# Kernel optimization log

Measured on AMD Instinct MI355X. Metric: run time of the kernel, lower is better.

## Reference

```python
import jax, jax.numpy as jnp
import numpy as np

T, B, D, H, NQ = 512, 256, 256, 256, 4  # note H == B is required by the original torch broadcasting


def setup_inputs() -> dict:
    key = jax.random.key(0)
    ks = jax.random.split(key, 9)
    inp = {"inputs": jax.random.normal(ks[0], (T, B, D), jnp.float32)}
    names = ["forget", "input", "update", "output"]
    for j, n in enumerate(names):
        inp[f"W_{n}"] = jax.random.normal(ks[1 + j], (NQ, D + H), jnp.float32) * 0.05
        inp[f"b_{n}"] = jnp.zeros((NQ,), jnp.float32)
        inp[f"phi_{n}"] = jax.random.uniform(ks[5 + j], (NQ,), jnp.float32, 0.0, 2.0 * np.pi)
    return inp


def _qgate(z, phi):
    # 4-qubit circuit on |0000>: RX(z_j) then trainable RX(phi_j) on each wire
    # (two RX on the same wire compose: angle theta_j = z_j + phi_j), then the
    # CNOT ring (0->1,1->2,2->3,3->0), then <Z_0>.
    # Heisenberg picture: conjugating Z_0 back through the CNOT ring gives
    # Z_0 -> Z_1 Z_2 Z_3, and on the product state <Z_j> = cos(theta_j), so
    # <Z_0> = cos(theta_1) * cos(theta_2) * cos(theta_3)  (wire 0 drops out).
    c = jnp.cos(z + phi)  # [B, 4]
    return c[:, 1] * c[:, 2] * c[:, 3]  # [B]


def reference(inputs, W_forget, b_forget, phi_forget, W_input, b_input, phi_input,
              W_update, b_update, phi_update, W_output, b_output, phi_output):
    bsz = inputs.shape[1]
    hx = jnp.zeros((bsz, H), inputs.dtype)
    cx = jnp.zeros((bsz, H), inputs.dtype)

    def step(carry, x):
        hx, cx = carry
        comb = jnp.concatenate([x, hx], axis=1)  # [B, D+H]
        f = jax.nn.sigmoid(_qgate(comb @ W_forget.T + b_forget, phi_forget))   # [B]
        i = jax.nn.sigmoid(_qgate(comb @ W_input.T + b_input, phi_input))      # [B]
        g = jnp.tanh(_qgate(comb @ W_update.T + b_update, phi_update))         # [B]
        o = jax.nn.sigmoid(_qgate(comb @ W_output.T + b_output, phi_output))   # [B]
        # [B] * [B,H] broadcasts the gate over the hidden axis (valid since H == B,
        # exactly matching the original torch semantics)
        cx = f * cx + i * g
        hx = o * jnp.tanh(cx)
        return (hx, cx), hx

    (hx, cx), outs = jax.lax.scan(step, (hx, cx), inputs)
    return outs, hx, cx
```

## Files before the change

kernel.cpp:

```cpp
#include <hip/hip_runtime.h>


#define T_DIM 512
#define B_DIM 256
#define D_DIM 256
#define H_DIM 256
#define DH    512
#define NG    16
#define XPAD  68
#define INV2PI 0.15915494309189535f

typedef float f32x4 __attribute__((ext_vector_type(4)));

#if __has_builtin(__builtin_amdgcn_fractf) && __has_builtin(__builtin_amdgcn_cosf)
#define TRIG_REV 1
#else
#define TRIG_REV 0
#endif

__device__ __forceinline__ float fast_sigmoid(float x) {
    return 1.0f / (1.0f + __expf(-x));
}
__device__ __forceinline__ float fast_tanh(float x) {
    float e = __expf(2.0f * x);
    return (e - 1.0f) / (e + 1.0f);
}
__device__ __forceinline__ float cos_rev(float x) {
#if TRIG_REV
    return __builtin_amdgcn_cosf(__builtin_amdgcn_fractf(x));
#else
    return __cosf(x * 6.283185307179586f);
#endif
}
template <int CTRL, int RM, int BM, bool BC>
__device__ __forceinline__ float dadd(float x) {
    return x + __int_as_float(
        __builtin_amdgcn_update_dpp(0, __float_as_int(x), CTRL, RM, BM, BC));
}
__device__ __forceinline__ float wsum(float x) {
    x = dadd<0x111, 0xf, 0xf, true >(x);
    x = dadd<0x112, 0xf, 0xf, true >(x);
    x = dadd<0x114, 0xf, 0xf, true >(x);
    x = dadd<0x118, 0xf, 0xf, true >(x);
    x = dadd<0x142, 0xa, 0xf, false>(x);
    x = dadd<0x143, 0xc, 0xf, false>(x);
    return x;
}
__device__ __forceinline__ float bcast63(float x) {
    return __int_as_float(__builtin_amdgcn_readlane(__float_as_int(x), 63));
}
__device__ __forceinline__ void lds_barrier() {
    __asm__ volatile("s_waitcnt lgkmcnt(0)\n\ts_barrier" ::: "memory");
}

__global__ __launch_bounds__(256) void zx_kernel(
    const float* __restrict__ x,
    const float* __restrict__ Wf, const float* __restrict__ Wi,
    const float* __restrict__ Wu, const float* __restrict__ Wo,
    const float* __restrict__ bf, const float* __restrict__ bi,
    const float* __restrict__ bu, const float* __restrict__ bo,
    const float* __restrict__ phf, const float* __restrict__ phi,
    const float* __restrict__ phu, const float* __restrict__ pho,
    float* __restrict__ zx)
{
    __shared__ float Xc[256][XPAD];
    __shared__ float Wc[NG][XPAD];
    const int tid = threadIdx.x;
    const int rt  = tid >> 2;
    const int qt  = tid & 3;

    const float* bv = (qt == 0) ? bf : (qt == 1) ? bi : (qt == 2) ? bu : bo;
    const float* pv = (qt == 0) ? phf : (qt == 1) ? phi : (qt == 2) ? phu : pho;
    float acc[4][4];
    #pragma unroll
    for (int j = 0; j < 4; ++j) {
        const float bj = bv[j] + pv[j];
        acc[0][j] = bj; acc[1][j] = bj; acc[2][j] = bj; acc[3][j] = bj;
    }

    const long base = (long)blockIdx.x * 256 * D_DIM;

    for (int c = 0; c < 4; ++c) {
        const int k0 = c * 64;
        #pragma unroll
        for (int it = 0; it < 16; ++it) {
            const int e = tid + it * 256;
            const int row = e >> 4, col4 = (e & 15) * 4;
            *(float4*)&Xc[row][col4] =
                *(const float4*)(x + base + (long)row * D_DIM + k0 + col4);
        }
        {
            const int q16 = tid >> 4, col4 = (tid & 15) * 4;
            const int g = q16 >> 2, qj = q16 & 3;
            const float* W = (g == 0) ? Wf : (g == 1) ? Wi : (g == 2) ? Wu : Wo;
            *(float4*)&Wc[q16][col4] = *(const float4*)(W + qj * DH + k0 + col4);
        }
        __syncthreads();

        #pragma unroll 4
        for (int kk = 0; kk < 16; ++kk) {
            const int k4 = kk * 4;
            float4 xv0 = *(float4*)&Xc[rt][k4];
            float4 xv1 = *(float4*)&Xc[rt +  64][k4];
            float4 xv2 = *(float4*)&Xc[rt + 128][k4];
            float4 xv3 = *(float4*)&Xc[rt + 192][k4];
            float4 wv0 = *(float4*)&Wc[4 * qt + 0][k4];
            float4 wv1 = *(float4*)&Wc[4 * qt + 1][k4];
            float4 wv2 = *(float4*)&Wc[4 * qt + 2][k4];
            float4 wv3 = *(float4*)&Wc[4 * qt + 3][k4];
            #pragma unroll
            for (int i = 0; i < 4; ++i) {
                const float4 xv = (i == 0) ? xv0 : (i == 1) ? xv1 : (i == 2) ? xv2 : xv3;
                acc[i][0] = fmaf(xv.x, wv0.x, fmaf(xv.y, wv0.y, fmaf(xv.z, wv0.z, fmaf(xv.w, wv0.w, acc[i][0]))));
                acc[i][1] = fmaf(xv.x, wv1.x, fmaf(xv.y, wv1.y, fmaf(xv.z, wv1.z, fmaf(xv.w, wv1.w, acc[i][1]))));
                acc[i][2] = fmaf(xv.x, wv2.x, fmaf(xv.y, wv2.y, fmaf(xv.z, wv2.z, fmaf(xv.w, wv2.w, acc[i][2]))));
                acc[i][3] = fmaf(xv.x, wv3.x, fmaf(xv.y, wv3.y, fmaf(xv.z, wv3.z, fmaf(xv.w, wv3.w, acc[i][3]))));
            }
        }
        __syncthreads();
    }

    const long orow = (long)blockIdx.x * 256;
    #pragma unroll
    for (int i = 0; i < 4; ++i) {
        *(float4*)&zx[(orow + rt + 64 * i) * NG + qt * 4] =
            make_float4(acc[i][0] * INV2PI, acc[i][1] * INV2PI,
                        acc[i][2] * INV2PI, acc[i][3] * INV2PI);
    }
}

__global__ __launch_bounds__(256) void rec_kernel(
    const float* __restrict__ Wf, const float* __restrict__ Wi,
    const float* __restrict__ Wu, const float* __restrict__ Wo,
    const float* __restrict__ zx,
    float* __restrict__ hv_tab,
    float* __restrict__ c_fin)
{
    __shared__ float Hbuf[2][H_DIM];
    const int tid  = threadIdx.x;
    const int lane = tid & 63;
    const int h    = tid;

    float4 W[12];
    #pragma unroll
    for (int c = 0; c < 12; ++c) {
        const int g = c / 3, j = c % 3 + 1;
        const float* Wg = (g == 0) ? Wf : (g == 1) ? Wi : (g == 2) ? Wu : Wo;
        float4 w = *(const float4*)(Wg + j * DH + 256 + 4 * lane);
        w.x *= INV2PI; w.y *= INV2PI; w.z *= INV2PI; w.w *= INV2PI;
        W[c] = w;
    }

    float C = 0.0f, Hprev = 0.0f;
    Hbuf[1][tid] = 0.0f;
    __syncthreads();

    float4 za0, za1, za2, za3, zb0, zb1, zb2, zb3;
    {
        const float4* p0 = (const float4*)(zx + (long)h * NG);
        const float4* p1 = (const float4*)(zx + ((long)B_DIM + h) * NG);
        za0 = p0[0]; za1 = p0[1]; za2 = p0[2]; za3 = p0[3];
        zb0 = p1[0]; zb1 = p1[1]; zb2 = p1[2]; zb3 = p1[3];
    }

    auto step = [&](int t, float4& z0, float4& z1, float4& z2, float4& z3) {
        const float4 Hv4 = *(const float4*)&Hbuf[(t + 1) & 1][4 * lane];
        hv_tab[(long)(t - 1) * H_DIM + h] = Hprev;

        float p[12];
        #pragma unroll
        for (int c = 0; c < 12; ++c)
            p[c] = fmaf(W[c].x, Hv4.x, fmaf(W[c].y, Hv4.y,
                       fmaf(W[c].z, Hv4.z, W[c].w * Hv4.w)));
        float zh[12];
        #pragma unroll
        for (int c = 0; c < 12; ++c) zh[c] = bcast63(wsum(p[c]));

        float4 n0, n1, n2, n3;
        {
            const int tp = (t + 2 < T_DIM) ? (t + 2) : t;
            const float4* pp = (const float4*)(zx + ((long)tp * B_DIM + h) * NG);
            n0 = pp[0]; n1 = pp[1]; n2 = pp[2]; n3 = pp[3];
        }

        const float f_ = fast_sigmoid(cos_rev(z0.y + zh[0]) * cos_rev(z0.z + zh[1])  * cos_rev(z0.w + zh[2]));
        const float i_ = fast_sigmoid(cos_rev(z1.y + zh[3]) * cos_rev(z1.z + zh[4])  * cos_rev(z1.w + zh[5]));
        const float g_ = fast_tanh   (cos_rev(z2.y + zh[6]) * cos_rev(z2.z + zh[7])  * cos_rev(z2.w + zh[8]));
        const float o_ = fast_sigmoid(cos_rev(z3.y + zh[9]) * cos_rev(z3.z + zh[10]) * cos_rev(z3.w + zh[11]));

        C = fmaf(f_, C, i_ * g_);
        const float Hnew = o_ * fast_tanh(C);
        Hbuf[t & 1][h] = Hnew;
        Hprev = Hnew;
        z0 = n0; z1 = n1; z2 = n2; z3 = n3;
        lds_barrier();
    };

    for (int t = 0; t < T_DIM; t += 2) {
        step(t,     za0, za1, za2, za3);
        step(t + 1, zb0, zb1, zb2, zb3);
    }

    hv_tab[(long)(T_DIM - 1) * H_DIM + h] = Hprev;
    c_fin[h] = C;
}

__global__ __launch_bounds__(256) void bc_kernel(
    const float* __restrict__ hv_tab, const float* __restrict__ c_fin,
    float* __restrict__ out)
{
    const int blk  = blockIdx.x;
    const int w    = threadIdx.x >> 6;
    const int lane = threadIdx.x & 63;

    const float* src;
    long base;
    int rbase;
    if (blk < 4 * T_DIM) {
        const int t = blk >> 2;
        rbase = (blk & 3) * 64;
        src = hv_tab + (long)t * H_DIM;
        base = (long)t * (B_DIM * H_DIM);
    } else {
        const int k = blk - 4 * T_DIM;
        rbase = (k & 3) * 64;
        src = (k < 4) ? (hv_tab + (long)(T_DIM - 1) * H_DIM) : c_fin;
        base = (long)T_DIM * (B_DIM * H_DIM) + (k < 4 ? 0 : (long)B_DIM * H_DIM);
    }
    const f32x4 v = ((const f32x4*)src)[lane];
    #pragma unroll
    for (int it = 0; it < 16; ++it) {
        const int row = rbase + w + 4 * it;
        __builtin_nontemporal_store(
            v, (f32x4*)(out + base + (long)row * H_DIM) + lane);
    }
}

extern "C" void kernel_launch(void* const* d_in, const int* in_sizes, int n_in,
                              void* d_out, int out_size, void* d_ws, size_t ws_size,
                              hipStream_t stream) {
    (void)in_sizes; (void)n_in; (void)out_size; (void)ws_size;
    const float* x   = (const float*)d_in[0];
    const float* Wf  = (const float*)d_in[1];
    const float* bf  = (const float*)d_in[2];
    const float* phf = (const float*)d_in[3];
    const float* Wi  = (const float*)d_in[4];
    const float* bi  = (const float*)d_in[5];
    const float* phi = (const float*)d_in[6];
    const float* Wu  = (const float*)d_in[7];
    const float* bu  = (const float*)d_in[8];
    const float* phu = (const float*)d_in[9];
    const float* Wo  = (const float*)d_in[10];
    const float* bo  = (const float*)d_in[11];
    const float* pho = (const float*)d_in[12];

    float* zx     = (float*)d_ws;
    float* hv_pad = zx + (size_t)T_DIM * B_DIM * NG;
    float* hv_tab = hv_pad + H_DIM;
    float* c_fin  = hv_tab + (size_t)T_DIM * H_DIM;

    zx_kernel<<<T_DIM, 256, 0, stream>>>(
        x, Wf, Wi, Wu, Wo, bf, bi, bu, bo, phf, phi, phu, pho, zx);

    rec_kernel<<<1, 256, 0, stream>>>(
        Wf, Wi, Wu, Wo, zx, hv_tab, c_fin);

    bc_kernel<<<4 * T_DIM + 8, 256, 0, stream>>>(hv_tab, c_fin, (float*)d_out);
}
```

Measured before the change: 639.3 us.

## Pack zx to 12 floats per row and split recurrence across 8 waves

The zx layout drops the unused wire-0 column, so each row holds 12 floats instead of 16. This cuts the bytes written by zx_kernel and the per-step prefetch in the recurrent kernel. The recurrent kernel now launches 512 threads (8 waves), and each wave owns 32 hidden units. The duplicated lanes still do the full 12 wave reductions over the hidden vector, so there are more waves to hide latency, at the cost of more barrier participants and redundant work.

```diff
diff --git a/kernel.cpp b/kernel.cpp
--- a/kernel.cpp
+++ b/kernel.cpp
@@ -7,6 +7,7 @@
 #define H_DIM 256
 #define DH    512
 #define NG    16
+#define NZ    12
 #define XPAD  68
 #define INV2PI 0.15915494309189535f
 
@@ -123,13 +124,14 @@
     const long orow = (long)blockIdx.x * 256;
     #pragma unroll
     for (int i = 0; i < 4; ++i) {
-        *(float4*)&zx[(orow + rt + 64 * i) * NG + qt * 4] =
-            make_float4(acc[i][0] * INV2PI, acc[i][1] * INV2PI,
-                        acc[i][2] * INV2PI, acc[i][3] * INV2PI);
-    }
-}
-
-__global__ __launch_bounds__(256) void rec_kernel(
+        const long off = (orow + rt + 64 * i) * NZ + qt * 3;
+        zx[off + 0] = acc[i][1] * INV2PI;
+        zx[off + 1] = acc[i][2] * INV2PI;
+        zx[off + 2] = acc[i][3] * INV2PI;
+    }
+}
+
+__global__ __launch_bounds__(512) void rec_kernel(
     const float* __restrict__ Wf, const float* __restrict__ Wi,
     const float* __restrict__ Wu, const float* __restrict__ Wo,
     const float* __restrict__ zx,
@@ -139,7 +141,9 @@
     __shared__ float Hbuf[2][H_DIM];
     const int tid  = threadIdx.x;
     const int lane = tid & 63;
-    const int h    = tid;
+    const int wv   = tid >> 6;
+    const int hh   = 32 * wv + (lane & 31);
+    const bool own = (lane < 32);
 
     float4 W[12];
     #pragma unroll
@@ -152,20 +156,20 @@
     }
 
     float C = 0.0f, Hprev = 0.0f;
-    Hbuf[1][tid] = 0.0f;
-    __syncthreads();
-
-    float4 za0, za1, za2, za3, zb0, zb1, zb2, zb3;
+    if (tid < H_DIM) Hbuf[1][tid] = 0.0f;
+    lds_barrier();
+
+    float4 za0, za1, za2, zb0, zb1, zb2;
     {
-        const float4* p0 = (const float4*)(zx + (long)h * NG);
-        const float4* p1 = (const float4*)(zx + ((long)B_DIM + h) * NG);
-        za0 = p0[0]; za1 = p0[1]; za2 = p0[2]; za3 = p0[3];
-        zb0 = p1[0]; zb1 = p1[1]; zb2 = p1[2]; zb3 = p1[3];
-    }
-
-    auto step = [&](int t, float4& z0, float4& z1, float4& z2, float4& z3) {
+        const float4* p0 = (const float4*)(zx + (long)hh * NZ);
+        const float4* p1 = (const float4*)(zx + ((long)B_DIM + hh) * NZ);
+        za0 = p0[0]; za1 = p0[1]; za2 = p0[2];
+        zb0 = p1[0]; zb1 = p1[1]; zb2 = p1[2];
+    }
+
+    auto step = [&](int t, float4& z0, float4& z1, float4& z2) {
         const float4 Hv4 = *(const float4*)&Hbuf[(t + 1) & 1][4 * lane];
-        hv_tab[(long)(t - 1) * H_DIM + h] = Hprev;
+        if (own) hv_tab[(long)(t - 1) * H_DIM + hh] = Hprev;
 
         float p[12];
         #pragma unroll
@@ -176,33 +180,33 @@
         #pragma unroll
         for (int c = 0; c < 12; ++c) zh[c] = bcast63(wsum(p[c]));
 
-        float4 n0, n1, n2, n3;
+        const float f_ = fast_sigmoid(cos_rev(z0.x + zh[0]) * cos_rev(z0.y + zh[1])  * cos_rev(z0.z + zh[2]));
+        const float i_ = fast_sigmoid(cos_rev(z0.w + zh[3]) * cos_rev(z1.x + zh[4])  * cos_rev(z1.y + zh[5]));
+        const float g_ = fast_tanh   (cos_rev(z1.z + zh[6]) * cos_rev(z1.w + zh[7])  * cos_rev(z2.x + zh[8]));
+        const float o_ = fast_sigmoid(cos_rev(z2.y + zh[9]) * cos_rev(z2.z + zh[10]) * cos_rev(z2.w + zh[11]));
+
         {
             const int tp = (t + 2 < T_DIM) ? (t + 2) : t;
-            const float4* pp = (const float4*)(zx + ((long)tp * B_DIM + h) * NG);
-            n0 = pp[0]; n1 = pp[1]; n2 = pp[2]; n3 = pp[3];
-        }
-
-        const float f_ = fast_sigmoid(cos_rev(z0.y + zh[0]) * cos_rev(z0.z + zh[1])  * cos_rev(z0.w + zh[2]));
-        const float i_ = fast_sigmoid(cos_rev(z1.y + zh[3]) * cos_rev(z1.z + zh[4])  * cos_rev(z1.w + zh[5]));
-        const float g_ = fast_tanh   (cos_rev(z2.y + zh[6]) * cos_rev(z2.z + zh[7])  * cos_rev(z2.w + zh[8]));
-        const float o_ = fast_sigmoid(cos_rev(z3.y + zh[9]) * cos_rev(z3.z + zh[10]) * cos_rev(z3.w + zh[11]));
+            const float4* pp = (const float4*)(zx + ((long)tp * B_DIM + hh) * NZ);
+            z0 = pp[0]; z1 = pp[1]; z2 = pp[2];
+        }
 
         C = fmaf(f_, C, i_ * g_);
         const float Hnew = o_ * fast_tanh(C);
-        Hbuf[t & 1][h] = Hnew;
+        if (own) Hbuf[t & 1][hh] = Hnew;
         Hprev = Hnew;
-        z0 = n0; z1 = n1; z2 = n2; z3 = n3;
         lds_barrier();
     };
 
     for (int t = 0; t < T_DIM; t += 2) {
-        step(t,     za0, za1, za2, za3);
-        step(t + 1, zb0, zb1, zb2, zb3);
-    }
-
-    hv_tab[(long)(T_DIM - 1) * H_DIM + h] = Hprev;
-    c_fin[h] = C;
+        step(t,     za0, za1, za2);
+        step(t + 1, zb0, zb1, zb2);
+    }
+
+    if (own) {
+        hv_tab[(long)(T_DIM - 1) * H_DIM + hh] = Hprev;
+        c_fin[hh] = C;
+    }
 }
 
 __global__ __launch_bounds__(256) void bc_kernel(
@@ -255,14 +259,14 @@
     const float* pho = (const float*)d_in[12];
 
     float* zx     = (float*)d_ws;
-    float* hv_pad = zx + (size_t)T_DIM * B_DIM * NG;
+    float* hv_pad = zx + (size_t)T_DIM * B_DIM * NZ;
     float* hv_tab = hv_pad + H_DIM;
     float* c_fin  = hv_tab + (size_t)T_DIM * H_DIM;
 
     zx_kernel<<<T_DIM, 256, 0, stream>>>(
         x, Wf, Wi, Wu, Wo, bf, bi, bu, bo, phf, phi, phu, pho, zx);
 
-    rec_kernel<<<1, 256, 0, stream>>>(
+    rec_kernel<<<1, 512, 0, stream>>>(
         Wf, Wi, Wu, Wo, zx, hv_tab, c_fin);
 
     bc_kernel<<<4 * T_DIM + 8, 256, 0, stream>>>(hv_tab, c_fin, (float*)d_out);
```

After: 886.1 us. 38.6% more time.
